# Performance work log

Hardware: AMD Instinct MI355X
Metric: run time of the kernel (lower is better)

## Reference

```python
import jax, jax.numpy as jnp
import numpy as np

NEG_SLOPE = 0.2  # PyG GATConv default leaky_relu slope
EPS = 1e-16


def setup_inputs() -> dict:
    key = jax.random.key(0)
    ks = jax.random.split(key, 8)
    N, E, F = 50000, 1600000, 128
    L, H, C = 3, 4, 32  # layers, heads, per-head channels; H*C == F
    Dh = 32             # MLP hidden (== hidden_channels)
    x = jax.random.normal(ks[0], (N, F), jnp.float32)
    edge_index = jax.random.randint(ks[1], (2, E), 0, N, jnp.int32)
    W = jax.random.normal(ks[2], (L, F, H * C), jnp.float32) * 0.1
    att_src = jax.random.normal(ks[3], (L, H, C), jnp.float32) * 0.1
    att_dst = jax.random.normal(ks[4], (L, H, C), jnp.float32) * 0.1
    b_conv = jnp.zeros((L, H * C), jnp.float32)
    W1 = jax.random.normal(ks[5], (F + H * C, Dh), jnp.float32) * 0.1
    b1 = jnp.zeros((Dh,), jnp.float32)
    W2 = jax.random.normal(ks[6], (Dh, 1), jnp.float32) * 0.1
    b2 = jnp.zeros((1,), jnp.float32)
    return {"x": x, "edge_index": edge_index, "W": W, "att_src": att_src,
            "att_dst": att_dst, "b_conv": b_conv, "W1": W1, "b1": b1,
            "W2": W2, "b2": b2}


def _gat_layer(x, src, dst, W, a_s, a_d, b, N):
    H, C = a_s.shape
    h = (x @ W).reshape(N, H, C)                      # [N,H,C]
    alpha_s = jnp.sum(h * a_s, axis=-1)               # [N,H]
    alpha_d = jnp.sum(h * a_d, axis=-1)               # [N,H]
    e = jax.nn.leaky_relu(alpha_s[src] + alpha_d[dst], NEG_SLOPE)  # [E,H]
    # segment softmax over incoming edges of each dst node
    m = jax.ops.segment_max(e, dst, num_segments=N)
    ex = jnp.exp(e - m[dst])
    s = jax.ops.segment_sum(ex, dst, num_segments=N)
    a = ex / (s[dst] + EPS)                           # [E,H]
    out = jax.ops.segment_sum(h[src] * a[:, :, None], dst, num_segments=N)
    return out.reshape(N, H * C) + b


def reference(x, edge_index, W, att_src, att_dst, b_conv, W1, b1, W2, b2):
    N = x.shape[0]
    loops = jnp.arange(N, dtype=edge_index.dtype)
    src = jnp.concatenate([edge_index[0], loops])  # PyG GATConv adds self loops
    dst = jnp.concatenate([edge_index[1], loops])
    x0 = x
    for l in range(W.shape[0]):
        x = _gat_layer(x, src, dst, W[l], att_src[l], att_dst[l], b_conv[l], N)
    h = jnp.concatenate([x, x0], axis=-1)
    h = jax.nn.relu(h @ W1 + b1)
    return jax.nn.sigmoid(h @ W2 + b2)
```

## Files before the change

kernel.cpp:

```cpp
#include <hip/hip_runtime.h>

#define NEG_SLOPE 0.2f
#define EPSF 1e-16f
#define SEG_SHIFT 13

typedef unsigned int uint;
typedef unsigned short ushort;
typedef __attribute__((ext_vector_type(8))) short short8;
typedef __attribute__((ext_vector_type(4))) float floatx4;
typedef __attribute__((ext_vector_type(4))) uint uintx4;
typedef __attribute__((ext_vector_type(2))) uint uintx2;

static __device__ __forceinline__ ushort f2bf(float f) {
    uint u = __float_as_uint(f);
    return (ushort)((u + 0x7FFFu + ((u >> 16) & 1u)) >> 16);
}
static __device__ __forceinline__ uint pack2(float a, float b) {
    return (uint)f2bf(a) | ((uint)f2bf(b) << 16);
}
static __device__ __forceinline__ float bf_lo(uint p) { return __uint_as_float(p << 16); }
static __device__ __forceinline__ float bf_hi(uint p) { return __uint_as_float(p & 0xFFFF0000u); }
static __device__ __forceinline__ short8 u2s8(uint4 v) {
    union { uint4 u; short8 s; } c; c.u = v; return c.s;
}
static __device__ __forceinline__ void load_lds16(const void* g, void* l) {
    __builtin_amdgcn_global_load_lds(
        (const __attribute__((address_space(1))) void*)g,
        (__attribute__((address_space(3))) void*)l, 16, 0, 0);
}

#define GA_LDS_BYTES (2048 * 16 + 16 * 65 * 16)

static __device__ __forceinline__ void gemm_body(
    char* smraw, const uint4* __restrict__ xb, const uint4* __restrict__ Wp,
    const float* __restrict__ att_s, const float* __restrict__ att_d,
    uint* __restrict__ h2, float* __restrict__ alpha_s,
    float* __restrict__ alpha_d, int N, int rowBase)
{
    uint4* sW = (uint4*)smraw;
    uint4* sX = sW + 2048;

    const int t = threadIdx.x;
    const int wb = t & ~63;

#pragma unroll
    for (int i = 0; i < 8; ++i)
        load_lds16(Wp + i * 256 + t, sW + i * 256 + wb);

#pragma unroll
    for (int i = 0; i < 4; ++i) {
        int f = t + i * 256;
        int row = f >> 4, c8 = f & 15;
        uint4 v = make_uint4(0u, 0u, 0u, 0u);
        if (rowBase + row < N) v = xb[(size_t)(rowBase + row) * 16 + c8];
        sX[c8 * 65 + row] = v;
    }
    __syncthreads();

    const int w = t >> 6, lane = t & 63, q = lane >> 4, l15 = lane & 15;
    short8 xf[4];
#pragma unroll
    for (int s = 0; s < 4; ++s)
        xf[s] = u2s8(sX[(4 * s + q) * 65 + 16 * w + l15]);

    floatx4 acc[8];
#pragma unroll
    for (int ct = 0; ct < 8; ++ct) acc[ct] = (floatx4){0.f, 0.f, 0.f, 0.f};
#pragma unroll
    for (int ct = 0; ct < 8; ++ct) {
#pragma unroll
        for (int s = 0; s < 4; ++s) {
            short8 wf = u2s8(sW[(4 * s + q) * 128 + 16 * ct + l15]);
            acc[ct] = __builtin_amdgcn_mfma_f32_16x16x32_bf16(wf, xf[s], acc[ct], 0, 0, 0);
        }
    }

    const int node = rowBase + 16 * w + l15;
    if (node < N) {
        uint2* hp = (uint2*)(h2 + (size_t)node * 64);
#pragma unroll
        for (int ct = 0; ct < 8; ++ct) {
            uint2 o;
            o.x = pack2(acc[ct][0], acc[ct][1]);
            o.y = pack2(acc[ct][2], acc[ct][3]);
            hp[4 * ct + q] = o;
        }
    }
    float ps[4], pd[4];
#pragma unroll
    for (int hd = 0; hd < 4; ++hd) {
        const float4 as0 = *(const float4*)(att_s + 32 * hd + 4 * q);
        const float4 as1 = *(const float4*)(att_s + 32 * hd + 16 + 4 * q);
        const float4 ad0 = *(const float4*)(att_d + 32 * hd + 4 * q);
        const float4 ad1 = *(const float4*)(att_d + 32 * hd + 16 + 4 * q);
        floatx4 c0 = acc[2 * hd], c1 = acc[2 * hd + 1];
        ps[hd] = c0[0] * as0.x + c0[1] * as0.y + c0[2] * as0.z + c0[3] * as0.w
               + c1[0] * as1.x + c1[1] * as1.y + c1[2] * as1.z + c1[3] * as1.w;
        pd[hd] = c0[0] * ad0.x + c0[1] * ad0.y + c0[2] * ad0.z + c0[3] * ad0.w
               + c1[0] * ad1.x + c1[1] * ad1.y + c1[2] * ad1.z + c1[3] * ad1.w;
    }
#pragma unroll
    for (int hd = 0; hd < 4; ++hd) {
        ps[hd] += __shfl_xor(ps[hd], 16);
        ps[hd] += __shfl_xor(ps[hd], 32);
        pd[hd] += __shfl_xor(pd[hd], 16);
        pd[hd] += __shfl_xor(pd[hd], 32);
    }
    if (node < N) {
        alpha_s[(size_t)node * 4 + q] = ps[q];
        alpha_d[(size_t)node * 4 + q] = pd[q];
    }
}

__global__ __launch_bounds__(256) void prep_count_kernel(
    const float* __restrict__ W, const float* __restrict__ W1,
    const float* __restrict__ x, uint4* __restrict__ Wp,
    uint4* __restrict__ W1p, uint4* __restrict__ xb,
    const int* __restrict__ ei, int E, int NB,
    int* __restrict__ bucket_count, int L, int N, int nbPrep)
{
    __shared__ int cnt[256];
    if ((int)blockIdx.x >= nbPrep) {
        cnt[threadIdx.x] = 0;
        __syncthreads();
        const int base = (blockIdx.x - nbPrep) * 2048 + threadIdx.x;
#pragma unroll
        for (int j = 0; j < 8; ++j) {
            int idx = base + j * 256;
            if (idx < E) atomicAdd(&cnt[ei[E + idx] >> 8], 1);
        }
        __syncthreads();
        int c = cnt[threadIdx.x];
        if ((int)threadIdx.x < NB && c) atomicAdd(&bucket_count[threadIdx.x], c);
        return;
    }
    int id = blockIdx.x * 256 + threadIdx.x;
    const int nW = L * 2048;
    const int nX = N * 16;
    if (id < nW) {
        int l = id >> 11, s = id & 2047;
        int chunk = s >> 7, col = s & 127;
        const float* wp = W + (size_t)l * 16384 + (chunk * 8) * 128 + col;
        uint4 pk;
        pk.x = pack2(wp[0],   wp[128]);
        pk.y = pack2(wp[256], wp[384]);
        pk.z = pack2(wp[512], wp[640]);
        pk.w = pack2(wp[768], wp[896]);
        Wp[id] = pk;
    } else if (id < nW + 1024) {
        int s = id - nW;
        int chunk = s >> 5, col = s & 31;
        const float* wp = W1 + (chunk * 8) * 32 + col;
        uint4 pk;
        pk.x = pack2(wp[0],   wp[32]);
        pk.y = pack2(wp[64],  wp[96]);
        pk.z = pack2(wp[128], wp[160]);
        pk.w = pack2(wp[192], wp[224]);
        W1p[s] = pk;
    } else if (id < nW + 1024 + nX) {
        int xid = id - nW - 1024;
        int row = xid >> 4, c8 = xid & 15;
        const float4* xp = (const float4*)(x + (size_t)row * 128 + c8 * 8);
        float4 v0 = xp[0], v1 = xp[1];
        uint4 pk;
        pk.x = pack2(v0.x, v0.y); pk.y = pack2(v0.z, v0.w);
        pk.z = pack2(v1.x, v1.y); pk.w = pack2(v1.z, v1.w);
        xb[xid] = pk;
    }
}

__global__ __launch_bounds__(256) void dist_gemm_kernel(
    const int* __restrict__ ei, int E, int NB,
    const int* __restrict__ bucket_count, int* __restrict__ bucket_cursor,
    uint* __restrict__ bdata, int nbEd,
    const uint4* __restrict__ xb, const uint4* __restrict__ Wp,
    const float* __restrict__ att_s, const float* __restrict__ att_d,
    uint* __restrict__ h2, float* __restrict__ alpha_s,
    float* __restrict__ alpha_d, int N)
{
    __shared__ __align__(16) char smraw[GA_LDS_BYTES];
    const int t = threadIdx.x;
    if ((int)blockIdx.x >= nbEd) {
        gemm_body(smraw, xb, Wp, att_s, att_d, h2, alpha_s, alpha_d, N,
                  (blockIdx.x - nbEd) * 64);
        return;
    }
    int* cnt = (int*)smraw;
    int* sc  = cnt + 256;
    int* bb  = sc + 256;
    cnt[t] = 0;
    __syncthreads();
    const int base = blockIdx.x * 2048 + t;
    int srcs[8], dsts[8], rank[8];
#pragma unroll
    for (int j = 0; j < 8; ++j) {
        int idx = base + j * 256;
        if (idx < E) {
            srcs[j] = ei[idx];
            dsts[j] = ei[E + idx];
            rank[j] = atomicAdd(&cnt[dsts[j] >> 8], 1);
        } else dsts[j] = -1;
    }
    __syncthreads();
    int bc = (t < NB) ? bucket_count[t] : 0;
    sc[t] = bc;
    __syncthreads();
    for (int off = 1; off < 256; off <<= 1) {
        int x = sc[t];
        int a = (t >= off) ? sc[t - off] : 0;
        __syncthreads();
        sc[t] = x + a;
        __syncthreads();
    }
    int gbase = sc[t] - bc;
    int c = cnt[t];
    bb[t] = (t < NB && c) ? (gbase + atomicAdd(&bucket_cursor[t], c)) : 0;
    __syncthreads();
#pragma unroll
    for (int j = 0; j < 8; ++j) {
        if (dsts[j] >= 0) {
            int b = dsts[j] >> 8;
            bdata[bb[b] + rank[j]] = (uint)srcs[j] | ((uint)(dsts[j] & 255) << 16);
        }
    }
}

#define BCAP 12800
__global__ __launch_bounds__(256) void bucket_csr_kernel(
    const uint* __restrict__ bdata, const int* __restrict__ bucket_count,
    int NB, int E, int* __restrict__ row_start, ushort* __restrict__ csr_src,
    int N)
{
    __shared__ int hist[2048];
    __shared__ int cur[2048];
    __shared__ int scn[256];
    __shared__ int sb[256];
    __shared__ ushort buf[BCAP];
    const int b = blockIdx.x;
    const int t = threadIdx.x;

    int bc = (t < NB) ? bucket_count[t] : 0;
    sb[t] = bc;
    __syncthreads();
    for (int off = 1; off < 256; off <<= 1) {
        int x = sb[t];
        int a = (t >= off) ? sb[t - off] : 0;
        __syncthreads();
        sb[t] = x + a;
        __syncthreads();
    }
    const int beg = (b > 0) ? sb[b - 1] : 0;
    const int sz = sb[b] - beg;
    if (b == 0 && t == 0) row_start[N] = E;

#pragma unroll
    for (int j = 0; j < 8; ++j) hist[t * 8 + j] = 0;
    __syncthreads();
    for (int i = t; i < sz; i += 256) {
        uint d = bdata[beg + i];
        int key = (int)((d >> 16) << 3) | (int)((d & 0xFFFFu) >> SEG_SHIFT);
        atomicAdd(&hist[key], 1);
    }
    __syncthreads();
    int local[8]; int s = 0;
#pragma unroll
    for (int j = 0; j < 8; ++j) { local[j] = hist[t * 8 + j]; s += local[j]; }
    scn[t] = s;
    __syncthreads();
    for (int off = 1; off < 256; off <<= 1) {
        int x = scn[t];
        int a = (t >= off) ? scn[t - off] : 0;
        __syncthreads();
        scn[t] = x + a;
        __syncthreads();
    }
    int run = scn[t] - s;
#pragma unroll
    for (int j = 0; j < 8; ++j) { cur[t * 8 + j] = run; run += local[j]; }
    __syncthreads();
    int node = b * 256 + t;
    if (node < N) row_start[node] = beg + cur[t << 3];
    __syncthreads();
    if (sz <= BCAP) {
        for (int i = t; i < sz; i += 256) {
            uint d = bdata[beg + i];
            int key = (int)((d >> 16) << 3) | (int)((d & 0xFFFFu) >> SEG_SHIFT);
            int pos = atomicAdd(&cur[key], 1);
            buf[pos] = (ushort)(d & 0xFFFFu);
        }
        __syncthreads();
        for (int i = t; i < sz; i += 256)
            __builtin_nontemporal_store(buf[i], &csr_src[beg + i]);
    } else {
        for (int i = t; i < sz; i += 256) {
            uint d = bdata[beg + i];
            int key = (int)((d >> 16) << 3) | (int)((d & 0xFFFFu) >> SEG_SHIFT);
            int pos = atomicAdd(&cur[key], 1);
            csr_src[beg + pos] = (ushort)(d & 0xFFFFu);
        }
    }
}

static __device__ __forceinline__ void agg_core(
    const ushort* __restrict__ csr_src, const int* __restrict__ row_start,
    const float* __restrict__ alpha_s, const float* __restrict__ alpha_d,
    const uint* __restrict__ h2, int g, int l, int head,
    float& a0, float& a1, float& a2, float& a3,
    float& a4, float& a5, float& a6, float& a7, float& sx)
{
    const char* hbase = (const char*)h2 + (size_t)l * 16;
    const float ad = alpha_d[g * 4 + head];

    float e = alpha_s[g * 4 + head] + ad;
    e = e > 0.f ? e : NEG_SLOPE * e;
    float ex = __expf(e);
    uint4 q = *(const uint4*)(hbase + (uint)g * 256u);
    a0 = ex * bf_lo(q.x); a1 = ex * bf_hi(q.x);
    a2 = ex * bf_lo(q.y); a3 = ex * bf_hi(q.y);
    a4 = ex * bf_lo(q.z); a5 = ex * bf_hi(q.z);
    a6 = ex * bf_lo(q.w); a7 = ex * bf_hi(q.w);
    sx = ex;

    const int beg = row_start[g];
    const int end = row_start[g + 1];
    int k = beg;
    for (; k + 4 <= end; k += 4) {
        uint s0 = csr_src[k], s1 = csr_src[k + 1];
        uint s2 = csr_src[k + 2], s3 = csr_src[k + 3];
        uint4 q0 = *(const uint4*)(hbase + s0 * 256u);
        uint4 q1 = *(const uint4*)(hbase + s1 * 256u);
        uint4 q2 = *(const uint4*)(hbase + s2 * 256u);
        uint4 q3 = *(const uint4*)(hbase + s3 * 256u);
        float e0 = alpha_s[s0 * 4 + head] + ad;
        float e1 = alpha_s[s1 * 4 + head] + ad;
        float e2 = alpha_s[s2 * 4 + head] + ad;
        float e3 = alpha_s[s3 * 4 + head] + ad;
        e0 = e0 > 0.f ? e0 : NEG_SLOPE * e0;
        e1 = e1 > 0.f ? e1 : NEG_SLOPE * e1;
        e2 = e2 > 0.f ? e2 : NEG_SLOPE * e2;
        e3 = e3 > 0.f ? e3 : NEG_SLOPE * e3;
        float x0 = __expf(e0), x1 = __expf(e1);
        float x2 = __expf(e2), x3 = __expf(e3);
        a0 += x0 * bf_lo(q0.x) + x1 * bf_lo(q1.x) + x2 * bf_lo(q2.x) + x3 * bf_lo(q3.x);
        a1 += x0 * bf_hi(q0.x) + x1 * bf_hi(q1.x) + x2 * bf_hi(q2.x) + x3 * bf_hi(q3.x);
        a2 += x0 * bf_lo(q0.y) + x1 * bf_lo(q1.y) + x2 * bf_lo(q2.y) + x3 * bf_lo(q3.y);
        a3 += x0 * bf_hi(q0.y) + x1 * bf_hi(q1.y) + x2 * bf_hi(q2.y) + x3 * bf_hi(q3.y);
        a4 += x0 * bf_lo(q0.z) + x1 * bf_lo(q1.z) + x2 * bf_lo(q2.z) + x3 * bf_lo(q3.z);
        a5 += x0 * bf_hi(q0.z) + x1 * bf_hi(q1.z) + x2 * bf_hi(q2.z) + x3 * bf_hi(q3.z);
        a6 += x0 * bf_lo(q0.w) + x1 * bf_lo(q1.w) + x2 * bf_lo(q2.w) + x3 * bf_lo(q3.w);
        a7 += x0 * bf_hi(q0.w) + x1 * bf_hi(q1.w) + x2 * bf_hi(q2.w) + x3 * bf_hi(q3.w);
        sx += x0 + x1 + x2 + x3;
    }
    for (; k < end; ++k) {
        uint s0 = csr_src[k];
        float e0 = alpha_s[s0 * 4 + head] + ad;
        uint4 q0 = *(const uint4*)(hbase + s0 * 256u);
        e0 = e0 > 0.f ? e0 : NEG_SLOPE * e0;
        float x0 = __expf(e0);
        a0 += x0 * bf_lo(q0.x); a1 += x0 * bf_hi(q0.x);
        a2 += x0 * bf_lo(q0.y); a3 += x0 * bf_hi(q0.y);
        a4 += x0 * bf_lo(q0.z); a5 += x0 * bf_hi(q0.z);
        a6 += x0 * bf_lo(q0.w); a7 += x0 * bf_hi(q0.w);
        sx += x0;
    }
}

__global__ __launch_bounds__(256) void aggemm_kernel(
    const ushort* __restrict__ csr_src, const int* __restrict__ row_start,
    const float* __restrict__ alpha_s, const float* __restrict__ alpha_d,
    const uint* __restrict__ h2in, const float* __restrict__ b,
    const uint4* __restrict__ Wnext,
    const float* __restrict__ att_s, const float* __restrict__ att_d,
    uint* __restrict__ h2out, float* __restrict__ alpha_s_out,
    float* __restrict__ alpha_d_out, int N)
{
    __shared__ __align__(16) uint4 tile[16 * 17];
    const int t = threadIdx.x;
    const int nodeBase = blockIdx.x * 16;
    const int gl = t >> 4;
    const int g = nodeBase + gl;
    const int l = t & 15;
    const bool active = g < N;

    uint4 o = make_uint4(0u, 0u, 0u, 0u);
    if (active) {
        float a0, a1, a2, a3, a4, a5, a6, a7, sx;
        agg_core(csr_src, row_start, alpha_s, alpha_d, h2in, g, l, l >> 2,
                 a0, a1, a2, a3, a4, a5, a6, a7, sx);
        const float inv = 1.f / (sx + EPSF);
        const float4 b0 = ((const float4*)b)[l * 2];
        const float4 b1 = ((const float4*)b)[l * 2 + 1];
        o.x = pack2(b0.x + a0 * inv, b0.y + a1 * inv);
        o.y = pack2(b0.z + a2 * inv, b0.w + a3 * inv);
        o.z = pack2(b1.x + a4 * inv, b1.y + a5 * inv);
        o.w = pack2(b1.z + a6 * inv, b1.w + a7 * inv);
    }
    tile[gl * 17 + l] = o;
    __syncthreads();

    const int w = t >> 6, lane = t & 63, q = lane >> 4, l15 = lane & 15;
    floatx4 acc0 = (floatx4){0.f, 0.f, 0.f, 0.f};
    floatx4 acc1 = (floatx4){0.f, 0.f, 0.f, 0.f};
#pragma unroll
    for (int s = 0; s < 4; ++s) {
        short8 xfr = u2s8(tile[l15 * 17 + 4 * s + q]);
        short8 wf0 = u2s8(Wnext[(4 * s + q) * 128 + 16 * (2 * w) + l15]);
        short8 wf1 = u2s8(Wnext[(4 * s + q) * 128 + 16 * (2 * w + 1) + l15]);
        acc0 = __builtin_amdgcn_mfma_f32_16x16x32_bf16(wf0, xfr, acc0, 0, 0, 0);
        acc1 = __builtin_amdgcn_mfma_f32_16x16x32_bf16(wf1, xfr, acc1, 0, 0, 0);
    }
    const int node = nodeBase + l15;
    if (node < N) {
        uint* hp = h2out + (size_t)node * 64;
        uintx2 o0, o1;
        o0.x = pack2(acc0[0], acc0[1]); o0.y = pack2(acc0[2], acc0[3]);
        o1.x = pack2(acc1[0], acc1[1]); o1.y = pack2(acc1[2], acc1[3]);
        __builtin_nontemporal_store(o0, (uintx2*)(hp + 16 * w + 2 * q));
        __builtin_nontemporal_store(o1, (uintx2*)(hp + 16 * w + 8 + 2 * q));
    }
    const float4 as0 = *(const float4*)(att_s + 32 * w + 4 * q);
    const float4 as1 = *(const float4*)(att_s + 32 * w + 16 + 4 * q);
    const float4 ad0 = *(const float4*)(att_d + 32 * w + 4 * q);
    const float4 ad1 = *(const float4*)(att_d + 32 * w + 16 + 4 * q);
    float ps = acc0[0] * as0.x + acc0[1] * as0.y + acc0[2] * as0.z + acc0[3] * as0.w
             + acc1[0] * as1.x + acc1[1] * as1.y + acc1[2] * as1.z + acc1[3] * as1.w;
    float pd = acc0[0] * ad0.x + acc0[1] * ad0.y + acc0[2] * ad0.z + acc0[3] * ad0.w
             + acc1[0] * ad1.x + acc1[1] * ad1.y + acc1[2] * ad1.z + acc1[3] * ad1.w;
    ps += __shfl_xor(ps, 16); ps += __shfl_xor(ps, 32);
    pd += __shfl_xor(pd, 16); pd += __shfl_xor(pd, 32);
    if (node < N && q == 0) {
        alpha_s_out[(size_t)node * 4 + w] = ps;
        alpha_d_out[(size_t)node * 4 + w] = pd;
    }
}

__global__ __launch_bounds__(256) void aggmlp_kernel(
    const ushort* __restrict__ csr_src, const int* __restrict__ row_start,
    const float* __restrict__ alpha_s, const float* __restrict__ alpha_d,
    const uint* __restrict__ h2in, const float* __restrict__ b,
    const uint4* __restrict__ xb0, const uint4* __restrict__ W1p,
    const float* __restrict__ b1, const float* __restrict__ W2,
    const float* __restrict__ b2, float* __restrict__ out, int N)
{
    __shared__ __align__(16) uint4 tile[16 * 33];
    __shared__ float pr[32];
    const int t = threadIdx.x;
    const int nodeBase = blockIdx.x * 16;
    const int gl = t >> 4;
    const int g = nodeBase + gl;
    const int l = t & 15;

    {
        uintx4 v = (uintx4){0u, 0u, 0u, 0u};
        if (g < N)
            v = __builtin_nontemporal_load(
                (const uintx4*)(xb0 + (size_t)g * 16 + l));
        union { uintx4 x; uint4 u; } cc; cc.x = v;
        tile[gl * 33 + 16 + l] = cc.u;
    }

    uint4 o = make_uint4(0u, 0u, 0u, 0u);
    if (g < N) {
        float a0, a1, a2, a3, a4, a5, a6, a7, sx;
        agg_core(csr_src, row_start, alpha_s, alpha_d, h2in, g, l, l >> 2,
                 a0, a1, a2, a3, a4, a5, a6, a7, sx);
        const float inv = 1.f / (sx + EPSF);
        const float4 b0 = ((const float4*)b)[l * 2];
        const float4 b1v = ((const float4*)b)[l * 2 + 1];
        o.x = pack2(b0.x + a0 * inv, b0.y + a1 * inv);
        o.y = pack2(b0.z + a2 * inv, b0.w + a3 * inv);
        o.z = pack2(b1v.x + a4 * inv, b1v.y + a5 * inv);
        o.w = pack2(b1v.z + a6 * inv, b1v.w + a7 * inv);
    }
    tile[gl * 33 + l] = o;
    __syncthreads();

    const int w = t >> 6, lane = t & 63, q = lane >> 4, l15 = lane & 15;
    if (w < 2) {
        floatx4 acc = (floatx4){0.f, 0.f, 0.f, 0.f};
#pragma unroll
        for (int s = 0; s < 8; ++s) {
            short8 a = u2s8(tile[l15 * 33 + 4 * s + q]);
            short8 bb = u2s8(W1p[(4 * s + q) * 32 + 16 * w + l15]);
            acc = __builtin_amdgcn_mfma_f32_16x16x32_bf16(a, bb, acc, 0, 0, 0);
        }
        const int col = 16 * w + l15;
        const float b1c = b1[col], w2c = W2[col];
#pragma unroll
        for (int r = 0; r < 4; ++r) {
            float v = acc[r] + b1c;
            v = v > 0.f ? v : 0.f;
            float p = v * w2c;
            p += __shfl_xor(p, 1);
            p += __shfl_xor(p, 2);
            p += __shfl_xor(p, 4);
            p += __shfl_xor(p, 8);
            if (l15 == 0) pr[w * 16 + 4 * q + r] = p;
        }
    }
    __syncthreads();
    if (t < 16) {
        int node = nodeBase + t;
        if (node < N) {
            float z = pr[t] + pr[16 + t] + b2[0];
            out[node] = 1.f / (1.f + __expf(-z));
        }
    }
}

extern "C" void kernel_launch(void* const* d_in, const int* in_sizes, int n_in,
                              void* d_out, int out_size, void* d_ws, size_t ws_size,
                              hipStream_t stream)
{
    const float* x       = (const float*)d_in[0];
    const int*   ei      = (const int*)d_in[1];
    const float* W       = (const float*)d_in[2];
    const float* att_src = (const float*)d_in[3];
    const float* att_dst = (const float*)d_in[4];
    const float* b_conv  = (const float*)d_in[5];
    const float* W1      = (const float*)d_in[6];
    const float* b1      = (const float*)d_in[7];
    const float* W2      = (const float*)d_in[8];
    const float* b2      = (const float*)d_in[9];
    float* outp = (float*)d_out;

    const int N = in_sizes[0] / 128;
    const int E = in_sizes[1] / 2;
    const int L = in_sizes[2] / (128 * 128);
    const int NB = (N + 255) >> 8;

    char* ws = (char*)d_ws;
    uint*  h2a      = (uint*)ws;
    uint*  h2b      = h2a + (size_t)N * 64;
    uint4* xb0      = (uint4*)(h2b + (size_t)N * 64);
    float* alphaA_s = (float*)(xb0 + (size_t)N * 16);
    float* alphaA_d = alphaA_s + (size_t)N * 4;
    float* alphaB_s = alphaA_d + (size_t)N * 4;
    float* alphaB_d = alphaB_s + (size_t)N * 4;
    uint4* Wp       = (uint4*)(alphaB_d + (size_t)N * 4);
    uint4* W1p      = Wp + (size_t)L * 2048;
    int* bucket_count  = (int*)(W1p + 1024);
    int* bucket_cursor = bucket_count + 256;
    int* row_start     = bucket_cursor + 256;
    uint* bdata        = (uint*)(row_start + N + 1);
    ushort* csr_src    = (ushort*)(bdata + E);

    const int nbEc = (E + 2047) / 2048;
    const int nbEd = (E + 2047) / 2048;
    const int gBlocks = (N + 63) / 64;
    const int aggBlocks = (N + 15) / 16;
    const int prepItems = L * 2048 + 1024 + N * 16;
    const int nbPrep = (prepItems + 255) / 256;

    (void)hipMemsetAsync(bucket_count, 0, 512 * sizeof(int), stream);

    prep_count_kernel<<<nbPrep + nbEc, 256, 0, stream>>>(
        W, W1, x, Wp, W1p, xb0, ei, E, NB, bucket_count, L, N, nbPrep);

    dist_gemm_kernel<<<nbEd + gBlocks, 256, 0, stream>>>(
        ei, E, NB, bucket_count, bucket_cursor, bdata, nbEd,
        xb0, Wp, att_src, att_dst, h2a, alphaA_s, alphaA_d, N);

    bucket_csr_kernel<<<NB, 256, 0, stream>>>(bdata, bucket_count, NB, E,
                                              row_start, csr_src, N);

    aggemm_kernel<<<aggBlocks, 256, 0, stream>>>(
        csr_src, row_start, alphaA_s, alphaA_d, h2a,
        b_conv + 0 * 128, Wp + (size_t)1 * 2048,
        att_src + (size_t)1 * 128, att_dst + (size_t)1 * 128,
        h2b, alphaB_s, alphaB_d, N);

    aggemm_kernel<<<aggBlocks, 256, 0, stream>>>(
        csr_src, row_start, alphaB_s, alphaB_d, h2b,
        b_conv + (size_t)1 * 128, Wp + (size_t)2 * 2048,
        att_src + (size_t)2 * 128, att_dst + (size_t)2 * 128,
        h2a, alphaA_s, alphaA_d, N);

    aggmlp_kernel<<<aggBlocks, 256, 0, stream>>>(
        csr_src, row_start, alphaA_s, alphaA_d, h2a,
        b_conv + (size_t)2 * 128, xb0, W1p, b1, W2, b2, outp, N);
}
```

Measured before the change: 328.0 us.

## Co-schedule layer-0 GEMM with bucket CSR build instead of edge distribution

The layer-0 feature GEMM blocks are moved out of the edge-distribution kernel and appended to the per-bucket CSR construction kernel. That kernel only has about one block per 256-node bucket, fewer than the number of CUs, so the extra GEMM blocks can fill idle compute units, and the distribution kernel becomes a lightweight standalone launch. The CSR path now carves its histograms and buffer out of the shared GEMM LDS region, which may change occupancy for both block types. Separately, the aggregation kernel's bf16 feature stores switch from nontemporal to ordinary stores, so the next layer can hit those features in cache.

```diff
diff --git a/kernel.cpp b/kernel.cpp
--- a/kernel.cpp
+++ b/kernel.cpp
@@ -9,7 +9,6 @@
 typedef __attribute__((ext_vector_type(8))) short short8;
 typedef __attribute__((ext_vector_type(4))) float floatx4;
 typedef __attribute__((ext_vector_type(4))) uint uintx4;
-typedef __attribute__((ext_vector_type(2))) uint uintx2;
 
 static __device__ __forceinline__ ushort f2bf(float f) {
     uint u = __float_as_uint(f);
@@ -169,25 +168,15 @@
     }
 }
 
-__global__ __launch_bounds__(256) void dist_gemm_kernel(
+__global__ __launch_bounds__(256) void dist_kernel(
     const int* __restrict__ ei, int E, int NB,
     const int* __restrict__ bucket_count, int* __restrict__ bucket_cursor,
-    uint* __restrict__ bdata, int nbEd,
-    const uint4* __restrict__ xb, const uint4* __restrict__ Wp,
-    const float* __restrict__ att_s, const float* __restrict__ att_d,
-    uint* __restrict__ h2, float* __restrict__ alpha_s,
-    float* __restrict__ alpha_d, int N)
-{
-    __shared__ __align__(16) char smraw[GA_LDS_BYTES];
+    uint* __restrict__ bdata)
+{
+    __shared__ int cnt[256];
+    __shared__ int sc[256];
+    __shared__ int bb[256];
     const int t = threadIdx.x;
-    if ((int)blockIdx.x >= nbEd) {
-        gemm_body(smraw, xb, Wp, att_s, att_d, h2, alpha_s, alpha_d, N,
-                  (blockIdx.x - nbEd) * 64);
-        return;
-    }
-    int* cnt = (int*)smraw;
-    int* sc  = cnt + 256;
-    int* bb  = sc + 256;
     cnt[t] = 0;
     __syncthreads();
     const int base = blockIdx.x * 2048 + t;
@@ -226,18 +215,27 @@
 }
 
 #define BCAP 12800
-__global__ __launch_bounds__(256) void bucket_csr_kernel(
+__global__ __launch_bounds__(256) void csr_gemm_kernel(
     const uint* __restrict__ bdata, const int* __restrict__ bucket_count,
     int NB, int E, int* __restrict__ row_start, ushort* __restrict__ csr_src,
-    int N)
-{
-    __shared__ int hist[2048];
-    __shared__ int cur[2048];
-    __shared__ int scn[256];
-    __shared__ int sb[256];
-    __shared__ ushort buf[BCAP];
+    const uint4* __restrict__ xb, const uint4* __restrict__ Wp,
+    const float* __restrict__ att_s, const float* __restrict__ att_d,
+    uint* __restrict__ h2, float* __restrict__ alpha_s,
+    float* __restrict__ alpha_d, int N)
+{
+    __shared__ __align__(16) char smraw[GA_LDS_BYTES];
+    const int t = threadIdx.x;
+    if ((int)blockIdx.x >= NB) {
+        gemm_body(smraw, xb, Wp, att_s, att_d, h2, alpha_s, alpha_d, N,
+                  (blockIdx.x - NB) * 64);
+        return;
+    }
+    int* hist = (int*)smraw;
+    int* cur  = hist + 2048;
+    int* scn  = cur + 2048;
+    int* sb   = scn + 256;
+    ushort* buf = (ushort*)(sb + 256);
     const int b = blockIdx.x;
-    const int t = threadIdx.x;
 
     int bc = (t < NB) ? bucket_count[t] : 0;
     sb[t] = bc;
@@ -411,12 +409,12 @@
     }
     const int node = nodeBase + l15;
     if (node < N) {
-        uint* hp = h2out + (size_t)node * 64;
-        uintx2 o0, o1;
+        uint2* hp = (uint2*)(h2out + (size_t)node * 64);
+        uint2 o0, o1;
         o0.x = pack2(acc0[0], acc0[1]); o0.y = pack2(acc0[2], acc0[3]);
         o1.x = pack2(acc1[0], acc1[1]); o1.y = pack2(acc1[2], acc1[3]);
-        __builtin_nontemporal_store(o0, (uintx2*)(hp + 16 * w + 2 * q));
-        __builtin_nontemporal_store(o1, (uintx2*)(hp + 16 * w + 8 + 2 * q));
+        hp[8 * w + q] = o0;
+        hp[8 * w + 4 + q] = o1;
     }
     const float4 as0 = *(const float4*)(att_s + 32 * w + 4 * q);
     const float4 as1 = *(const float4*)(att_s + 32 * w + 16 + 4 * q);
@@ -545,8 +543,7 @@
     uint* bdata        = (uint*)(row_start + N + 1);
     ushort* csr_src    = (ushort*)(bdata + E);
 
-    const int nbEc = (E + 2047) / 2048;
-    const int nbEd = (E + 2047) / 2048;
+    const int nbE = (E + 2047) / 2048;
     const int gBlocks = (N + 63) / 64;
     const int aggBlocks = (N + 15) / 16;
     const int prepItems = L * 2048 + 1024 + N * 16;
@@ -554,15 +551,15 @@
 
     (void)hipMemsetAsync(bucket_count, 0, 512 * sizeof(int), stream);
 
-    prep_count_kernel<<<nbPrep + nbEc, 256, 0, stream>>>(
+    prep_count_kernel<<<nbPrep + nbE, 256, 0, stream>>>(
         W, W1, x, Wp, W1p, xb0, ei, E, NB, bucket_count, L, N, nbPrep);
 
-    dist_gemm_kernel<<<nbEd + gBlocks, 256, 0, stream>>>(
-        ei, E, NB, bucket_count, bucket_cursor, bdata, nbEd,
+    dist_kernel<<<nbE, 256, 0, stream>>>(ei, E, NB, bucket_count,
+                                         bucket_cursor, bdata);
+
+    csr_gemm_kernel<<<NB + gBlocks, 256, 0, stream>>>(
+        bdata, bucket_count, NB, E, row_start, csr_src,
         xb0, Wp, att_src, att_dst, h2a, alphaA_s, alphaA_d, N);
-
-    bucket_csr_kernel<<<NB, 256, 0, stream>>>(bdata, bucket_count, NB, E,
-                                              row_start, csr_src, N);
 
     aggemm_kernel<<<aggBlocks, 256, 0, stream>>>(
         csr_src, row_start, alphaA_s, alphaA_d, h2a,
```

Result: no change. 323.2 us (-1.5%).
